# Performance work log

Hardware: AMD Instinct MI355X
Metric: run time of the kernel (lower is better)

## Reference

```python
import jax, jax.numpy as jnp
import numpy as np

N = 50000          # total_nodes (B*N diagonal-stacked graphs)
E = 800000         # total edges (avg degree 16)
HID = 128          # hidden_size
HEADS = 8          # num_heads


def setup_inputs() -> dict:
    key = jax.random.key(0)
    ks = jax.random.split(key, 10)
    s = 1.0 / np.sqrt(HID)
    x = jax.random.normal(ks[0], (N, HID), jnp.float32)
    edge_index = jax.random.randint(ks[1], (2, E), 0, N, dtype=jnp.int32).astype(jnp.int64)
    Wq = jax.random.normal(ks[2], (HID, HID), jnp.float32) * s
    bq = jax.random.normal(ks[3], (HID,), jnp.float32) * 0.01
    Wk = jax.random.normal(ks[4], (HID, HID), jnp.float32) * s
    bk = jax.random.normal(ks[5], (HID,), jnp.float32) * 0.01
    Wv = jax.random.normal(ks[6], (HID, HID), jnp.float32) * s
    bv = jax.random.normal(ks[7], (HID,), jnp.float32) * 0.01
    Wo = jax.random.normal(ks[8], (HID, HID), jnp.float32) * s
    bo = jax.random.normal(ks[9], (HID,), jnp.float32) * 0.01
    return {"x": x, "edge_index": edge_index, "total_nodes": N,
            "Wq": Wq, "bq": bq, "Wk": Wk, "bk": bk,
            "Wv": Wv, "bv": bv, "Wo": Wo, "bo": bo}


def reference(x, edge_index, total_nodes, Wq, bq, Wk, bk, Wv, bv, Wo, bo):
    H = HEADS
    D = HID // HEADS
    scale = D ** (-0.5)
    # torch Linear: y = x @ W.T + b
    Q = (x @ Wq.T + bq).reshape(-1, H, D)   # (N, H, D)
    K = (x @ Wk.T + bk).reshape(-1, H, D)
    V = (x @ Wv.T + bv).reshape(-1, H, D)
    src = edge_index[0]
    dst = edge_index[1]
    # edge-wise dot-product scores: (E, H)
    scores = jnp.einsum('ehd,ehd->eh', Q[dst], K[src]) * scale
    # scatter-softmax over edges sharing the same dst node
    mx = jax.ops.segment_max(scores, dst, num_segments=total_nodes)      # (N, H)
    ex = jnp.exp(scores - mx[dst])                                        # (E, H)
    se = jax.ops.segment_sum(ex, dst, num_segments=total_nodes)          # (N, H)
    attn = ex / (se[dst] + 1e-12)                                         # (E, H)
    # weighted message aggregation
    msg = attn[..., None] * V[src]                                        # (E, H, D)
    out = jax.ops.segment_sum(msg, dst, num_segments=total_nodes)        # (N, H, D)
    out = out.reshape(total_nodes, HID)
    return out @ Wo.T + bo
```

## Files before the change

### kernel.cpp

```cpp
#include <hip/hip_runtime.h>
#include <math.h>

#define NNODES 50000
#define NEDGES 800000
#define HIDDEN 128
#define NH 8
#define CAP 64
#define NPART 8
#define PART_SZ 6250
#define SCAT_BPP 128
#define SCAT_BLOCKS (NPART * SCAT_BPP)
#define QKV_WAVES 1563
#define QKV_BLOCKS 391

typedef __bf16 bf16x8 __attribute__((ext_vector_type(8)));
typedef float  f32x4  __attribute__((ext_vector_type(4)));

__device__ inline unsigned short f2b(float f) {
    unsigned u = __float_as_uint(f);
    unsigned r = (u + 0x7fffu + ((u >> 16) & 1u)) >> 16;
    return (unsigned short)r;
}

__device__ inline bf16x8 ld_a8(const float* __restrict__ p) {
    float4 a = *(const float4*)p;
    float4 b = *(const float4*)(p + 4);
    bf16x8 r;
    r[0] = (__bf16)a.x; r[1] = (__bf16)a.y; r[2] = (__bf16)a.z; r[3] = (__bf16)a.w;
    r[4] = (__bf16)b.x; r[5] = (__bf16)b.y; r[6] = (__bf16)b.z; r[7] = (__bf16)b.w;
    return r;
}

__global__ __launch_bounds__(256)
void pack_init(const float* __restrict__ Wq, const float* __restrict__ Wk,
               const float* __restrict__ Wv, const float* __restrict__ Wo,
               unsigned short* __restrict__ Pqkv, unsigned short* __restrict__ Po,
               int* __restrict__ cnt)
{
    if (blockIdx.x >= 32) {
        const int idx = (blockIdx.x - 32) * 256 + threadIdx.x;
        if (idx < NNODES / 4) ((int4*)cnt)[idx] = make_int4(0, 0, 0, 0);
        return;
    }
    const int s = blockIdx.x * 4 + (threadIdx.x >> 6);
    const int lane = threadIdx.x & 63;
    const float* W; unsigned short* P; int ct, c;
    if (s < 96) { ct = s >> 2; c = s & 3;
        W = (ct < 8) ? Wq : (ct < 16) ? Wk : Wv;
        P = Pqkv + (size_t)s * 512;
        ct &= 7;
    } else { int t = s - 96; ct = t >> 2; c = t & 3; W = Wo; P = Po + (size_t)t * 512; }
    const int colin = ct * 16 + (lane & 15);
    const int k0 = c * 32 + (lane >> 4) * 8;
    const float* sp = W + (size_t)colin * 128 + k0;
    unsigned short v[8];
#pragma unroll
    for (int j = 0; j < 8; ++j) v[j] = f2b(sp[j]);
    uint4 o;
    o.x = (unsigned)v[0] | ((unsigned)v[1] << 16);
    o.y = (unsigned)v[2] | ((unsigned)v[3] << 16);
    o.z = (unsigned)v[4] | ((unsigned)v[5] << 16);
    o.w = (unsigned)v[6] | ((unsigned)v[7] << 16);
    *(uint4*)(P + lane * 8) = o;
}

__global__ __launch_bounds__(256)
void qkv_scatter(const float* __restrict__ x, const unsigned short* __restrict__ Pqkv,
                 const float* __restrict__ bq, const float* __restrict__ bk,
                 const float* __restrict__ bv,
                 const int* __restrict__ src, const int* __restrict__ dst,
                 unsigned short* __restrict__ Qb, unsigned short* __restrict__ KVb,
                 int* __restrict__ cnt, int* __restrict__ bucket)
{
    if (blockIdx.x >= QKV_BLOCKS) {
        const int sb = blockIdx.x - QKV_BLOCKS;
        const int part = sb & (NPART - 1);
        const int blk  = sb >> 3;
        const int lo = part * PART_SZ, hi = lo + PART_SZ;
        for (int e = blk * 256 + threadIdx.x; e < NEDGES; e += SCAT_BPP * 256) {
            const int d = dst[e];
            if (d >= lo && d < hi) {
                const int pos = atomicAdd(&cnt[d], 1);
                if (pos < CAP) bucket[d * CAP + pos] = src[e];
            }
        }
        return;
    }

    const int w = blockIdx.x * 4 + (threadIdx.x >> 6);
    if (w >= QKV_WAVES) return;
    const int lane = threadIdx.x & 63;
    const int row0 = w * 32;
    const int ar = lane & 15, kg = lane >> 4;
    const bool two = (row0 + 16) < NNODES;

    const float* ap0 = x + (size_t)(row0 + ar) * 128 + kg * 8;
    const float* ap1 = two ? (ap0 + 16 * 128) : ap0;
    const bf16x8 a00 = ld_a8(ap0), a01 = ld_a8(ap0 + 32), a02 = ld_a8(ap0 + 64), a03 = ld_a8(ap0 + 96);
    const bf16x8 a10 = ld_a8(ap1), a11 = ld_a8(ap1 + 32), a12 = ld_a8(ap1 + 64), a13 = ld_a8(ap1 + 96);

    const unsigned short* wp = Pqkv + lane * 8;

#pragma unroll
    for (int t = 0; t < 8; ++t) {
        const unsigned short* bb = wp + (size_t)t * 2048;
        const bf16x8 b0 = *(const bf16x8*)(bb);
        const bf16x8 b1 = *(const bf16x8*)(bb + 512);
        const bf16x8 b2 = *(const bf16x8*)(bb + 1024);
        const bf16x8 b3 = *(const bf16x8*)(bb + 1536);

        f32x4 acc0 = {0.f, 0.f, 0.f, 0.f};
        f32x4 acc1 = {0.f, 0.f, 0.f, 0.f};
        acc0 = __builtin_amdgcn_mfma_f32_16x16x32_bf16(a00, b0, acc0, 0, 0, 0);
        acc1 = __builtin_amdgcn_mfma_f32_16x16x32_bf16(a10, b0, acc1, 0, 0, 0);
        acc0 = __builtin_amdgcn_mfma_f32_16x16x32_bf16(a01, b1, acc0, 0, 0, 0);
        acc1 = __builtin_amdgcn_mfma_f32_16x16x32_bf16(a11, b1, acc1, 0, 0, 0);
        acc0 = __builtin_amdgcn_mfma_f32_16x16x32_bf16(a02, b2, acc0, 0, 0, 0);
        acc1 = __builtin_amdgcn_mfma_f32_16x16x32_bf16(a12, b2, acc1, 0, 0, 0);
        acc0 = __builtin_amdgcn_mfma_f32_16x16x32_bf16(a03, b3, acc0, 0, 0, 0);
        acc1 = __builtin_amdgcn_mfma_f32_16x16x32_bf16(a13, b3, acc1, 0, 0, 0);

        const int colin = t * 16 + ar;
        const float bsc = bq[colin];
#pragma unroll
        for (int j = 0; j < 4; ++j)
            Qb[(size_t)(row0 + kg * 4 + j) * 128 + colin] = f2b(acc0[j] + bsc);
        if (two) {
#pragma unroll
            for (int j = 0; j < 4; ++j)
                Qb[(size_t)(row0 + 16 + kg * 4 + j) * 128 + colin] = f2b(acc1[j] + bsc);
        }
    }

#pragma unroll
    for (int tc = 0; tc < 8; ++tc) {
        const unsigned short* bbk = wp + (size_t)(8 + tc) * 2048;
        const unsigned short* bbv = wp + (size_t)(16 + tc) * 2048;
        const bf16x8 k0 = *(const bf16x8*)(bbk);
        const bf16x8 k1 = *(const bf16x8*)(bbk + 512);
        const bf16x8 k2 = *(const bf16x8*)(bbk + 1024);
        const bf16x8 k3 = *(const bf16x8*)(bbk + 1536);
        const bf16x8 v0 = *(const bf16x8*)(bbv);
        const bf16x8 v1 = *(const bf16x8*)(bbv + 512);
        const bf16x8 v2 = *(const bf16x8*)(bbv + 1024);
        const bf16x8 v3 = *(const bf16x8*)(bbv + 1536);

        f32x4 aK0 = {0.f, 0.f, 0.f, 0.f}, aK1 = aK0, aV0 = aK0, aV1 = aK0;
        aK0 = __builtin_amdgcn_mfma_f32_16x16x32_bf16(a00, k0, aK0, 0, 0, 0);
        aV0 = __builtin_amdgcn_mfma_f32_16x16x32_bf16(a00, v0, aV0, 0, 0, 0);
        aK1 = __builtin_amdgcn_mfma_f32_16x16x32_bf16(a10, k0, aK1, 0, 0, 0);
        aV1 = __builtin_amdgcn_mfma_f32_16x16x32_bf16(a10, v0, aV1, 0, 0, 0);
        aK0 = __builtin_amdgcn_mfma_f32_16x16x32_bf16(a01, k1, aK0, 0, 0, 0);
        aV0 = __builtin_amdgcn_mfma_f32_16x16x32_bf16(a01, v1, aV0, 0, 0, 0);
        aK1 = __builtin_amdgcn_mfma_f32_16x16x32_bf16(a11, k1, aK1, 0, 0, 0);
        aV1 = __builtin_amdgcn_mfma_f32_16x16x32_bf16(a11, v1, aV1, 0, 0, 0);
        aK0 = __builtin_amdgcn_mfma_f32_16x16x32_bf16(a02, k2, aK0, 0, 0, 0);
        aV0 = __builtin_amdgcn_mfma_f32_16x16x32_bf16(a02, v2, aV0, 0, 0, 0);
        aK1 = __builtin_amdgcn_mfma_f32_16x16x32_bf16(a12, k2, aK1, 0, 0, 0);
        aV1 = __builtin_amdgcn_mfma_f32_16x16x32_bf16(a12, v2, aV1, 0, 0, 0);
        aK0 = __builtin_amdgcn_mfma_f32_16x16x32_bf16(a03, k3, aK0, 0, 0, 0);
        aV0 = __builtin_amdgcn_mfma_f32_16x16x32_bf16(a03, v3, aV0, 0, 0, 0);
        aK1 = __builtin_amdgcn_mfma_f32_16x16x32_bf16(a13, k3, aK1, 0, 0, 0);
        aV1 = __builtin_amdgcn_mfma_f32_16x16x32_bf16(a13, v3, aV1, 0, 0, 0);

        const int colin = tc * 16 + ar;
        const float bkc = bk[colin], bvc = bv[colin];
        const int qoff = (colin >> 1) * 4;
        const bool store_lane = !(ar & 1);

#pragma unroll
        for (int j = 0; j < 4; ++j) {
            const unsigned kb = f2b(aK0[j] + bkc);
            const unsigned vb = f2b(aV0[j] + bvc);
            const unsigned ko = (unsigned)__shfl_xor((int)kb, 1) & 0xffffu;
            const unsigned vo = (unsigned)__shfl_xor((int)vb, 1) & 0xffffu;
            if (store_lane) {
                uint2 wq = { kb | (ko << 16), vb | (vo << 16) };
                *(uint2*)(KVb + (size_t)(row0 + kg * 4 + j) * 256 + qoff) = wq;
            }
        }
        if (two) {
#pragma unroll
            for (int j = 0; j < 4; ++j) {
                const unsigned kb = f2b(aK1[j] + bkc);
                const unsigned vb = f2b(aV1[j] + bvc);
                const unsigned ko = (unsigned)__shfl_xor((int)kb, 1) & 0xffffu;
                const unsigned vo = (unsigned)__shfl_xor((int)vb, 1) & 0xffffu;
                if (store_lane) {
                    uint2 wq = { kb | (ko << 16), vb | (vo << 16) };
                    *(uint2*)(KVb + (size_t)(row0 + 16 + kg * 4 + j) * 256 + qoff) = wq;
                }
            }
        }
    }
}

__global__ __launch_bounds__(256)
void fused_attn_kernel(const unsigned short* __restrict__ Qb,
                       const unsigned short* __restrict__ KVb,
                       const int* __restrict__ cnt, const int* __restrict__ bucket,
                       unsigned short* __restrict__ accumb)
{
    const int wave = threadIdx.x >> 6;
    const int lane = threadIdx.x & 63;
    const int n = blockIdx.x * 4 + wave;
    if (n >= NNODES) return;

    int deg = cnt[n];
    deg = deg > CAP ? CAP : deg;
    const int mysrc = (lane < deg) ? bucket[n * CAP + lane] : 0;

    const unsigned short* kvbase = KVb + lane * 4;

    const unsigned qw = *(const unsigned*)(Qb + (size_t)n * HIDDEN + lane * 2);
    const float qx = __uint_as_float(qw << 16) * 0.25f;
    const float qy = __uint_as_float(qw & 0xffff0000u) * 0.25f;

    float m = -INFINITY, s = 0.f, ox = 0.f, oy = 0.f;

    uint2 kvA = make_uint2(0,0), kvB = kvA, kvC = kvA, kvD = kvA;
    if (deg > 0) kvA = *(const uint2*)(kvbase + ((size_t)__shfl(mysrc, 0) << 8));
    if (deg > 1) kvB = *(const uint2*)(kvbase + ((size_t)__shfl(mysrc, 1) << 8));
    if (deg > 2) kvC = *(const uint2*)(kvbase + ((size_t)__shfl(mysrc, 2) << 8));
    if (deg > 3) kvD = *(const uint2*)(kvbase + ((size_t)__shfl(mysrc, 3) << 8));

    int i = 0;
    for (; i + 2 <= deg; i += 2) {
        const uint2 c0 = kvA, c1 = kvB;
        kvA = kvC; kvB = kvD;
        if (i + 4 < deg) kvC = *(const uint2*)(kvbase + ((size_t)__shfl(mysrc, i + 4) << 8));
        if (i + 5 < deg) kvD = *(const uint2*)(kvbase + ((size_t)__shfl(mysrc, i + 5) << 8));

        float d0 = qx * __uint_as_float(c0.x << 16) + qy * __uint_as_float(c0.x & 0xffff0000u);
        float d1 = qx * __uint_as_float(c1.x << 16) + qy * __uint_as_float(c1.x & 0xffff0000u);
        d0 += __shfl_xor(d0, 1);  d1 += __shfl_xor(d1, 1);
        d0 += __shfl_xor(d0, 2);  d1 += __shfl_xor(d1, 2);
        d0 += __shfl_xor(d0, 4);  d1 += __shfl_xor(d1, 4);

        const float pm = fmaxf(d0, d1);
        const float ee = __expf(-fabsf(d0 - d1));
        const bool g = d0 >= d1;
        const float v0x = __uint_as_float(c0.y << 16), v0y = __uint_as_float(c0.y & 0xffff0000u);
        const float v1x = __uint_as_float(c1.y << 16), v1y = __uint_as_float(c1.y & 0xffff0000u);
        const float sp  = 1.f + ee;
        const float ovx = fmaf(ee, g ? v1x : v0x, g ? v0x : v1x);
        const float ovy = fmaf(ee, g ? v1y : v0y, g ? v0y : v1y);

        const float dd = pm - m;
        const float em = __expf(-fabsf(dd));
        const bool nm = dd > 0.f;
        const float so = nm ? em : 1.f;
        const float sn = nm ? 1.f : em;
        m = nm ? pm : m;
        s  = fmaf(s,  so, sp  * sn);
        ox = fmaf(ox, so, ovx * sn);
        oy = fmaf(oy, so, ovy * sn);
    }
    if (i < deg) {
        const uint2 c0 = kvA;
        float d0 = qx * __uint_as_float(c0.x << 16) + qy * __uint_as_float(c0.x & 0xffff0000u);
        d0 += __shfl_xor(d0, 1);
        d0 += __shfl_xor(d0, 2);
        d0 += __shfl_xor(d0, 4);
        const float vx = __uint_as_float(c0.y << 16), vy = __uint_as_float(c0.y & 0xffff0000u);
        const float dd = d0 - m;
        const float em = __expf(-fabsf(dd));
        const bool nm = dd > 0.f;
        const float so = nm ? em : 1.f;
        const float pp = nm ? 1.f : em;
        m = nm ? d0 : m;
        s  = fmaf(s,  so, pp);
        ox = fmaf(ox, so, pp * vx);
        oy = fmaf(oy, so, pp * vy);
    }
    const float inv = 1.f / (s + 1e-12f);
    ushort2 ob = { f2b(ox * inv), f2b(oy * inv) };
    *(ushort2*)(accumb + (size_t)n * HIDDEN + lane * 2) = ob;
}

__global__ __launch_bounds__(256)
void outproj_mfma(const unsigned short* __restrict__ accumb, const unsigned short* __restrict__ Po,
                  const float* __restrict__ bo, float* __restrict__ out)
{
    const int band = blockIdx.x * 4 + (threadIdx.x >> 6);
    if (band >= 3125) return;
    const int lane = threadIdx.x & 63;
    const int row0 = band * 16;
    const int ar = lane & 15, kg = lane >> 4;

    const unsigned short* ab = accumb + (size_t)(row0 + ar) * 128 + kg * 8;
    const bf16x8 a0 = *(const bf16x8*)(ab);
    const bf16x8 a1 = *(const bf16x8*)(ab + 32);
    const bf16x8 a2 = *(const bf16x8*)(ab + 64);
    const bf16x8 a3 = *(const bf16x8*)(ab + 96);

    const unsigned short* wp = Po + lane * 8;
    bf16x8 pb0 = *(const bf16x8*)(wp);
    bf16x8 pb1 = *(const bf16x8*)(wp + 512);
    bf16x8 pb2 = *(const bf16x8*)(wp + 1024);
    bf16x8 pb3 = *(const bf16x8*)(wp + 1536);

#pragma unroll
    for (int t = 0; t < 8; ++t) {
        const bf16x8 b0 = pb0, b1 = pb1, b2 = pb2, b3 = pb3;
        if (t < 7) {
            const unsigned short* nw = wp + (size_t)(t + 1) * 2048;
            pb0 = *(const bf16x8*)(nw);
            pb1 = *(const bf16x8*)(nw + 512);
            pb2 = *(const bf16x8*)(nw + 1024);
            pb3 = *(const bf16x8*)(nw + 1536);
        }
        f32x4 acc = {0.f, 0.f, 0.f, 0.f};
        acc = __builtin_amdgcn_mfma_f32_16x16x32_bf16(a0, b0, acc, 0, 0, 0);
        acc = __builtin_amdgcn_mfma_f32_16x16x32_bf16(a1, b1, acc, 0, 0, 0);
        acc = __builtin_amdgcn_mfma_f32_16x16x32_bf16(a2, b2, acc, 0, 0, 0);
        acc = __builtin_amdgcn_mfma_f32_16x16x32_bf16(a3, b3, acc, 0, 0, 0);

        const int colin = t * 16 + ar;
        const float bsc = bo[colin];
#pragma unroll
        for (int j = 0; j < 4; ++j)
            out[(size_t)(row0 + kg * 4 + j) * 128 + colin] = acc[j] + bsc;
    }
}

extern "C" void kernel_launch(void* const* d_in, const int* in_sizes, int n_in,
                              void* d_out, int out_size, void* d_ws, size_t ws_size,
                              hipStream_t stream) {
    const float* x  = (const float*)d_in[0];
    const int*   ei = (const int*)d_in[1];
    const int*   src = ei;
    const int*   dst = ei + NEDGES;
    const float* Wq = (const float*)d_in[3];
    const float* bq = (const float*)d_in[4];
    const float* Wk = (const float*)d_in[5];
    const float* bk = (const float*)d_in[6];
    const float* Wv = (const float*)d_in[7];
    const float* bv = (const float*)d_in[8];
    const float* Wo = (const float*)d_in[9];
    const float* bo = (const float*)d_in[10];
    float* out = (float*)d_out;

    char* ws = (char*)d_ws;
    size_t off = 0;
    const size_t sz_nhb = (size_t)NNODES * HIDDEN * sizeof(unsigned short);
    unsigned short* Qb     = (unsigned short*)(ws + off); off += sz_nhb;
    unsigned short* KVb    = (unsigned short*)(ws + off); off += 2 * sz_nhb;
    unsigned short* accumb = (unsigned short*)(ws + off); off += sz_nhb;
    unsigned short* Pqkv   = (unsigned short*)(ws + off); off += 96 * 512 * sizeof(unsigned short);
    unsigned short* Po     = (unsigned short*)(ws + off); off += 32 * 512 * sizeof(unsigned short);
    int*            cnt    = (int*)(ws + off);            off += (size_t)NNODES * sizeof(int);
    int*            bucket = (int*)(ws + off);            off += (size_t)NNODES * CAP * sizeof(int);

    pack_init<<<81, 256, 0, stream>>>(Wq, Wk, Wv, Wo, Pqkv, Po, cnt);

    qkv_scatter<<<QKV_BLOCKS + SCAT_BLOCKS, 256, 0, stream>>>(
        x, Pqkv, bq, bk, bv, src, dst, Qb, KVb, cnt, bucket);

    fused_attn_kernel<<<(NNODES + 3) / 4, 256, 0, stream>>>(Qb, KVb, cnt, bucket, accumb);

    outproj_mfma<<<782, 256, 0, stream>>>(accumb, Po, bo, out);
}
```

Baseline: 131.8 us.

## Pack Q stores into 8-byte writes with permuted layout and schedule scatter blocks first

Q output stores change from scattered 2-byte writes to 8-byte packed writes. Adjacent columns are combined with lane shuffles, and pairs of column tiles are interleaved into a permuted per-row layout. The attention kernel's Q load uses a matching permuted offset, so each lane still reads the right pair of dims. Scatter blocks are also moved to the front of the grid so the edge bucketing work starts earlier. This adds shuffle work and a non-obvious Q layout that both kernels must keep in sync.

Measured after the change: 147.8 us. 1.12x slower.

```diff
diff --git a/kernel.cpp b/kernel.cpp
--- a/kernel.cpp
+++ b/kernel.cpp
@@ -72,8 +72,8 @@
                  unsigned short* __restrict__ Qb, unsigned short* __restrict__ KVb,
                  int* __restrict__ cnt, int* __restrict__ bucket)
 {
-    if (blockIdx.x >= QKV_BLOCKS) {
-        const int sb = blockIdx.x - QKV_BLOCKS;
+    if (blockIdx.x < SCAT_BLOCKS) {
+        const int sb = blockIdx.x;
         const int part = sb & (NPART - 1);
         const int blk  = sb >> 3;
         const int lo = part * PART_SZ, hi = lo + PART_SZ;
@@ -87,12 +87,13 @@
         return;
     }
 
-    const int w = blockIdx.x * 4 + (threadIdx.x >> 6);
+    const int w = (blockIdx.x - SCAT_BLOCKS) * 4 + (threadIdx.x >> 6);
     if (w >= QKV_WAVES) return;
     const int lane = threadIdx.x & 63;
     const int row0 = w * 32;
     const int ar = lane & 15, kg = lane >> 4;
     const bool two = (row0 + 16) < NNODES;
+    const bool sl = !(ar & 1);
 
     const float* ap0 = x + (size_t)(row0 + ar) * 128 + kg * 8;
     const float* ap1 = two ? (ap0 + 16 * 128) : ap0;
@@ -101,6 +102,7 @@
 
     const unsigned short* wp = Pqkv + lane * 8;
 
+    unsigned qst0[4], qst1[4];
 #pragma unroll
     for (int t = 0; t < 8; ++t) {
         const unsigned short* bb = wp + (size_t)t * 2048;
@@ -122,13 +124,33 @@
 
         const int colin = t * 16 + ar;
         const float bsc = bq[colin];
-#pragma unroll
-        for (int j = 0; j < 4; ++j)
-            Qb[(size_t)(row0 + kg * 4 + j) * 128 + colin] = f2b(acc0[j] + bsc);
-        if (two) {
-#pragma unroll
-            for (int j = 0; j < 4; ++j)
-                Qb[(size_t)(row0 + 16 + kg * 4 + j) * 128 + colin] = f2b(acc1[j] + bsc);
+        if ((t & 1) == 0) {
+#pragma unroll
+            for (int j = 0; j < 4; ++j) {
+                const unsigned a = f2b(acc0[j] + bsc);
+                const unsigned an = (unsigned)__shfl_xor((int)a, 1) & 0xffffu;
+                qst0[j] = a | (an << 16);
+                const unsigned c = f2b(acc1[j] + bsc);
+                const unsigned cn = (unsigned)__shfl_xor((int)c, 1) & 0xffffu;
+                qst1[j] = c | (cn << 16);
+            }
+        } else {
+            const int qoff = (t >> 1) * 32 + (ar >> 1) * 4;
+#pragma unroll
+            for (int j = 0; j < 4; ++j) {
+                const unsigned a = f2b(acc0[j] + bsc);
+                const unsigned an = (unsigned)__shfl_xor((int)a, 1) & 0xffffu;
+                if (sl) {
+                    uint2 wq = { qst0[j], a | (an << 16) };
+                    *(uint2*)(Qb + (size_t)(row0 + kg * 4 + j) * 128 + qoff) = wq;
+                }
+                const unsigned c = f2b(acc1[j] + bsc);
+                const unsigned cn = (unsigned)__shfl_xor((int)c, 1) & 0xffffu;
+                if (sl && two) {
+                    uint2 wq = { qst1[j], c | (cn << 16) };
+                    *(uint2*)(Qb + (size_t)(row0 + 16 + kg * 4 + j) * 128 + qoff) = wq;
+                }
+            }
         }
     }
 
@@ -166,7 +188,6 @@
         const int colin = tc * 16 + ar;
         const float bkc = bk[colin], bvc = bv[colin];
         const int qoff = (colin >> 1) * 4;
-        const bool store_lane = !(ar & 1);
 
 #pragma unroll
         for (int j = 0; j < 4; ++j) {
@@ -174,7 +195,7 @@
             const unsigned vb = f2b(aV0[j] + bvc);
             const unsigned ko = (unsigned)__shfl_xor((int)kb, 1) & 0xffffu;
             const unsigned vo = (unsigned)__shfl_xor((int)vb, 1) & 0xffffu;
-            if (store_lane) {
+            if (sl) {
                 uint2 wq = { kb | (ko << 16), vb | (vo << 16) };
                 *(uint2*)(KVb + (size_t)(row0 + kg * 4 + j) * 256 + qoff) = wq;
             }
@@ -186,7 +207,7 @@
                 const unsigned vb = f2b(aV1[j] + bvc);
                 const unsigned ko = (unsigned)__shfl_xor((int)kb, 1) & 0xffffu;
                 const unsigned vo = (unsigned)__shfl_xor((int)vb, 1) & 0xffffu;
-                if (store_lane) {
+                if (sl) {
                     uint2 wq = { kb | (ko << 16), vb | (vo << 16) };
                     *(uint2*)(KVb + (size_t)(row0 + 16 + kg * 4 + j) * 256 + qoff) = wq;
                 }
@@ -212,7 +233,8 @@
 
     const unsigned short* kvbase = KVb + lane * 4;
 
-    const unsigned qw = *(const unsigned*)(Qb + (size_t)n * HIDDEN + lane * 2);
+    const int qoff = ((lane >> 4) << 5) + ((lane & 7) << 2) + (((lane >> 3) & 1) << 1);
+    const unsigned qw = *(const unsigned*)(Qb + (size_t)n * HIDDEN + qoff);
     const float qx = __uint_as_float(qw << 16) * 0.25f;
     const float qy = __uint_as_float(qw & 0xffff0000u) * 0.25f;
 
@@ -354,7 +376,7 @@
 
     pack_init<<<81, 256, 0, stream>>>(Wq, Wk, Wv, Wo, Pqkv, Po, cnt);
 
-    qkv_scatter<<<QKV_BLOCKS + SCAT_BLOCKS, 256, 0, stream>>>(
+    qkv_scatter<<<SCAT_BLOCKS + QKV_BLOCKS, 256, 0, stream>>>(
         x, Pqkv, bq, bk, bv, src, dst, Qb, KVb, cnt, bucket);
 
     fused_attn_kernel<<<(NNODES + 3) / 4, 256, 0, stream>>>(Qb, KVb, cnt, bucket, accumb);
```
